# Kernel tuning notes

Measured on AMD Instinct MI355X. Metric: run time of the kernel, lower is better.

## Reference

```python
import jax, jax.numpy as jnp
import numpy as np

BLOCK = 64  # bnb 4-bit quant block size along the input dim

def dequant4bit(q, scale):
    # q: [out, in] int codes in [0,16); scale: [out, in//BLOCK]
    # symmetric 4-bit dequant: w = (code - 7.5) * blockwise scale
    return (q.astype(jnp.float32) - 7.5) * jnp.repeat(scale, BLOCK, axis=1)

def setup_inputs() -> dict:
    key = jax.random.key(0)
    ks = jax.random.split(key, 11)
    B, S, D, H, R = 4, 2048, 2048, 8192, 16
    return {
        "x1": jax.random.normal(ks[0], (B, S, D), jnp.float32),
        "w_up_q": jax.random.randint(ks[1], (H, D), 0, 16, dtype=jnp.int32),
        "w_up_scale": jax.random.uniform(ks[2], (H, D // BLOCK), jnp.float32) * 0.02,
        "b_up": jax.random.normal(ks[3], (H,), jnp.float32) * 0.01,
        "w_up_lora_a": jax.random.normal(ks[4], (D, R), jnp.float32) * 0.02,
        "w_up_lora_b": jax.random.normal(ks[5], (R, H), jnp.float32) * 0.02,
        "w_down_q": jax.random.randint(ks[6], (D, H), 0, 16, dtype=jnp.int32),
        "w_down_scale": jax.random.uniform(ks[7], (D, H // BLOCK), jnp.float32) * 0.02,
        "b_down": jax.random.normal(ks[8], (D,), jnp.float32) * 0.01,
        "w_down_lora_a": jax.random.normal(ks[9], (H, R), jnp.float32) * 0.02,
        "w_down_lora_b": jax.random.normal(ks[10], (R, D), jnp.float32) * 0.02,
    }

def reference(x1, w_up_q, w_up_scale, b_up, w_up_lora_a, w_up_lora_b,
              w_down_q, w_down_scale, b_down, w_down_lora_a, w_down_lora_b):
    # up projection: dequant-matmul + bias + LoRA (activation_forward='relu')
    w_up = dequant4bit(w_up_q, w_up_scale).T            # [D, H]
    y1 = x1 @ w_up + b_up + (x1 @ w_up_lora_a) @ w_up_lora_b   # [B, S, H]
    x2 = jax.nn.relu(y1)
    # down projection: dequant-matmul + bias + LoRA
    w_down = dequant4bit(w_down_q, w_down_scale).T      # [H, D]
    y2 = x2 @ w_down + b_down + (x2 @ w_down_lora_a) @ w_down_lora_b  # [B, S, D]
    return y2
```

## Files before the change

### kernel.cpp

```cpp
#include <hip/hip_runtime.h>
#include <hip/hip_bf16.h>
#include <stdint.h>
#include <stddef.h>

typedef __bf16 bf16;
typedef bf16  bf16x4 __attribute__((ext_vector_type(4)));
typedef bf16  bf16x8 __attribute__((ext_vector_type(8)));
typedef float f32x4  __attribute__((ext_vector_type(4)));

__device__ __forceinline__ void async_copy16(bf16* lds, const bf16* g) {
    __builtin_amdgcn_global_load_lds(
        (const __attribute__((address_space(1))) void*)g,
        (__attribute__((address_space(3))) void*)lds,
        16, 0, 0);
}

__device__ __forceinline__ void bar() { __builtin_amdgcn_s_barrier(); }
#define SFENCE() __builtin_amdgcn_sched_barrier(0)
#define WAIT_VM6()   do { asm volatile("s_waitcnt vmcnt(6)");   SFENCE(); } while (0)
#define WAIT_VM0()   do { asm volatile("s_waitcnt vmcnt(0)");   SFENCE(); } while (0)

__global__ __launch_bounds__(256) void cast_f32_to_bf16(
        const float* __restrict__ in, bf16* __restrict__ out, int n4) {
    int i = blockIdx.x * blockDim.x + threadIdx.x;
    if (i >= n4) return;
    const float4 v = *(const float4*)(in + (size_t)i * 4);
    bf16x4 o;
    o[0] = (bf16)v.x; o[1] = (bf16)v.y; o[2] = (bf16)v.z; o[3] = (bf16)v.w;
    *(bf16x4*)(out + (size_t)i * 4) = o;
}

__global__ __launch_bounds__(256) void dequant_lora(
        const int*   __restrict__ q,
        const float* __restrict__ scale,
        const float* __restrict__ A,
        const float* __restrict__ Bm,
        bf16* __restrict__ out,
        int N, int K) {
    const int tid = threadIdx.x;
    const int k0 = blockIdx.x * 64;
    const int n0 = blockIdx.y * 64;
    const int kk = k0 + (tid & 15) * 4;
    const int nb = n0 + (tid >> 4) * 4;

    f32x4 Ar[4][4];
    #pragma unroll
    for (int i = 0; i < 4; ++i)
        #pragma unroll
        for (int rq = 0; rq < 4; ++rq)
            Ar[i][rq] = *(const f32x4*)&A[(size_t)(kk + i) * 16 + rq * 4];
    f32x4 Br[16];
    #pragma unroll
    for (int r = 0; r < 16; ++r)
        Br[r] = *(const f32x4*)&Bm[(size_t)r * N + nb];

    const int scol = (unsigned)k0 >> 6;
    #pragma unroll
    for (int nn = 0; nn < 4; ++nn) {
        const int n = nb + nn;
        const int4 qv = *(const int4*)&q[(size_t)n * K + kk];
        const float s = scale[(size_t)n * (K >> 6) + scol];
        float l0 = 0.f, l1 = 0.f, l2 = 0.f, l3 = 0.f;
        #pragma unroll
        for (int r = 0; r < 16; ++r) {
            const float bv = Br[r][nn];
            l0 += Ar[0][r >> 2][r & 3] * bv;
            l1 += Ar[1][r >> 2][r & 3] * bv;
            l2 += Ar[2][r >> 2][r & 3] * bv;
            l3 += Ar[3][r >> 2][r & 3] * bv;
        }
        bf16x4 o;
        o[0] = (bf16)(((float)qv.x - 7.5f) * s + l0);
        o[1] = (bf16)(((float)qv.y - 7.5f) * s + l1);
        o[2] = (bf16)(((float)qv.z - 7.5f) * s + l2);
        o[3] = (bf16)(((float)qv.w - 7.5f) * s + l3);
        *(bf16x4*)&out[(size_t)n * K + kk] = o;
    }
}

template <bool RELU, typename OUT_T>
__global__ __launch_bounds__(512, 2) void gemm_bt256(
        const bf16* __restrict__ A, const bf16* __restrict__ B,
        const float* __restrict__ bias, OUT_T* __restrict__ C,
        int M, int N, int K) {
    __shared__ __attribute__((aligned(16))) bf16 As0[2][8192];
    __shared__ __attribute__((aligned(16))) bf16 As1[2][8192];
    __shared__ __attribute__((aligned(16))) bf16 Bs0[2][8192];
    __shared__ __attribute__((aligned(16))) bf16 Bs1[2][8192];

    const int tid  = threadIdx.x;
    const int wave = tid >> 6;
    const int lane = tid & 63;
    const int wm   = wave >> 2;
    const int wn   = wave & 3;
    const int bn   = blockIdx.x;
    const int bm   = blockIdx.y;

    const int srow = tid >> 3;
    const int scol = ((tid & 7) ^ (srow & 7)) * 8;
    const bf16* gA = A + ((size_t)(bm * 256) + srow) * K + scol;
    const bf16* gB = B + ((size_t)(bn * 256) + srow) * K + scol;

    auto stage2 = [&](bf16* halfBase, const bf16* g) {
        bf16* l = halfBase + wave * 512;
        async_copy16(l, g);
        async_copy16(l + 4096, g + (size_t)64 * K);
    };

    const int fr  = lane & 15;
    const int kq  = lane >> 4;
    const int cg0 = ((kq    ) ^ (fr & 7)) * 8;
    const int cg1 = ((kq + 4) ^ (fr & 7)) * 8;
    const int ra  = fr * 64;
    const int rb  = (wn & 1) * 4096 + fr * 64;

    f32x4 acc[8][4];
    #pragma unroll
    for (int i = 0; i < 8; ++i)
        #pragma unroll
        for (int j = 0; j < 4; ++j) {
            f32x4 z = {0.f, 0.f, 0.f, 0.f};
            acc[i][j] = z;
        }

    stage2(&Bs0[0][0], gB);
    stage2(&Bs0[1][0], gB + (size_t)128 * K);
    stage2(&As0[0][0], gA);
    stage2(&As0[1][0], gA + (size_t)128 * K);
    stage2(&Bs1[0][0], gB + 64);
    stage2(&Bs1[1][0], gB + (size_t)128 * K + 64);
    stage2(&As1[0][0], gA + 64);
    WAIT_VM6();
    bar();

    const int NT = K >> 6;
    bf16x8 fa[4][2], fb[4][2];

    for (int t0 = 0; t0 < NT; t0 += 2) {
        #pragma unroll
        for (int u = 0; u < 2; ++u) {
            const int t = t0 + u;
            bf16 (*AsC)[8192] = u ? As1 : As0;
            bf16 (*AsN)[8192] = u ? As0 : As1;
            bf16 (*BsC)[8192] = u ? Bs1 : Bs0;
            const bf16* aC = &AsC[wm][0];
            const bf16* bC = &BsC[wn >> 1][0];

            #pragma unroll
            for (int i = 0; i < 4; ++i) {
                fa[i][0] = *(const bf16x8*)(aC + i * 1024 + ra + cg0);
                fa[i][1] = *(const bf16x8*)(aC + i * 1024 + ra + cg1);
            }
            #pragma unroll
            for (int j = 0; j < 4; ++j) {
                fb[j][0] = *(const bf16x8*)(bC + rb + j * 1024 + cg0);
                fb[j][1] = *(const bf16x8*)(bC + rb + j * 1024 + cg1);
            }
            if (t + 1 < NT)
                stage2(&AsN[1][0], gA + (size_t)128 * K + (size_t)(t + 1) * 64);
            bar();
            __builtin_amdgcn_s_setprio(1);
            #pragma unroll
            for (int ks = 0; ks < 2; ++ks)
                #pragma unroll
                for (int i = 0; i < 4; ++i)
                    #pragma unroll
                    for (int j = 0; j < 2; ++j)
                        acc[i][j] = __builtin_amdgcn_mfma_f32_16x16x32_bf16(
                            fa[i][ks], fb[j][ks], acc[i][j], 0, 0, 0);
            __builtin_amdgcn_s_setprio(0);
            bar();

            if (t + 2 < NT)
                stage2(&BsC[0][0], gB + (size_t)(t + 2) * 64);
            bar();
            __builtin_amdgcn_s_setprio(1);
            #pragma unroll
            for (int ks = 0; ks < 2; ++ks)
                #pragma unroll
                for (int i = 0; i < 4; ++i)
                    #pragma unroll
                    for (int j = 2; j < 4; ++j)
                        acc[i][j] = __builtin_amdgcn_mfma_f32_16x16x32_bf16(
                            fa[i][ks], fb[j][ks], acc[i][j], 0, 0, 0);
            __builtin_amdgcn_s_setprio(0);
            bar();

            #pragma unroll
            for (int i = 0; i < 4; ++i) {
                fa[i][0] = *(const bf16x8*)(aC + (i + 4) * 1024 + ra + cg0);
                fa[i][1] = *(const bf16x8*)(aC + (i + 4) * 1024 + ra + cg1);
            }
            if (t + 2 < NT)
                stage2(&BsC[1][0], gB + (size_t)128 * K + (size_t)(t + 2) * 64);
            bar();
            __builtin_amdgcn_s_setprio(1);
            #pragma unroll
            for (int ks = 0; ks < 2; ++ks)
                #pragma unroll
                for (int i = 0; i < 4; ++i)
                    #pragma unroll
                    for (int j = 2; j < 4; ++j)
                        acc[i + 4][j] = __builtin_amdgcn_mfma_f32_16x16x32_bf16(
                            fa[i][ks], fb[j][ks], acc[i + 4][j], 0, 0, 0);
            __builtin_amdgcn_s_setprio(0);
            bar();

            if (t + 2 < NT) {
                stage2(&AsC[0][0], gA + (size_t)(t + 2) * 64);
                WAIT_VM6();
            } else {
                WAIT_VM0();
            }
            bar();
            __builtin_amdgcn_s_setprio(1);
            #pragma unroll
            for (int ks = 0; ks < 2; ++ks)
                #pragma unroll
                for (int i = 0; i < 4; ++i)
                    #pragma unroll
                    for (int j = 0; j < 2; ++j)
                        acc[i + 4][j] = __builtin_amdgcn_mfma_f32_16x16x32_bf16(
                            fa[i][ks], fb[j][ks], acc[i + 4][j], 0, 0, 0);
            __builtin_amdgcn_s_setprio(0);
            bar();
        }
    }

    const int er = bm * 256 + wm * 128 + (lane >> 4) * 4;
    const int ec = bn * 256 + wn * 64 + fr;
    #pragma unroll
    for (int j = 0; j < 4; ++j) {
        const int col = ec + j * 16;
        const float bv = bias[col];
        #pragma unroll
        for (int i = 0; i < 8; ++i) {
            #pragma unroll
            for (int r = 0; r < 4; ++r) {
                const int row = er + i * 16 + r;
                float v = acc[i][j][r] + bv;
                if (RELU) v = v > 0.f ? v : 0.f;
                C[(size_t)row * N + col] = (OUT_T)v;
            }
        }
    }
}

extern "C" void kernel_launch(void* const* d_in, const int* in_sizes, int n_in,
                              void* d_out, int out_size, void* d_ws, size_t ws_size,
                              hipStream_t stream) {
    const float* x1           = (const float*)d_in[0];
    const int*   w_up_q       = (const int*)  d_in[1];
    const float* w_up_scale   = (const float*)d_in[2];
    const float* b_up         = (const float*)d_in[3];
    const float* w_up_lora_a  = (const float*)d_in[4];
    const float* w_up_lora_b  = (const float*)d_in[5];
    const int*   w_down_q     = (const int*)  d_in[6];
    const float* w_down_scale = (const float*)d_in[7];
    const float* b_down       = (const float*)d_in[8];
    const float* w_down_lora_a= (const float*)d_in[9];
    const float* w_down_lora_b= (const float*)d_in[10];
    float* out = (float*)d_out;

    const int M = 8192, D = 2048, H = 8192;

    char* ws = (char*)d_ws;
    bf16* x1b = (bf16*)ws;
    bf16* wup = (bf16*)(ws + (size_t)M * D * 2);
    bf16* x2  = (bf16*)(ws + (size_t)M * D * 2 + (size_t)H * D * 2);
    bf16* wdn = x1b;

    {
        int n4 = (M * D) / 4;
        cast_f32_to_bf16<<<dim3((n4 + 255) / 256), dim3(256), 0, stream>>>(x1, x1b, n4);
    }
    dequant_lora<<<dim3(D / 64, H / 64), dim3(256), 0, stream>>>(
        w_up_q, w_up_scale, w_up_lora_a, w_up_lora_b, wup, H, D);
    gemm_bt256<true, bf16><<<dim3(H / 256, M / 256), dim3(512), 0, stream>>>(
        x1b, wup, b_up, x2, M, H, D);
    dequant_lora<<<dim3(H / 64, D / 64), dim3(256), 0, stream>>>(
        w_down_q, w_down_scale, w_down_lora_a, w_down_lora_b, wdn, D, H);
    gemm_bt256<false, float><<<dim3(D / 256, M / 256), dim3(512), 0, stream>>>(
        x2, wdn, b_down, out, M, D, H);
}
```

Measured before the change: 757.6 us.

## Restructure GEMM main loop to split K-halves and prefetch next tile fragments

Reorganizes the 8-wave MFMA main loop so each phase computes a full 4x4 sub-block for one K half (cg0 or cg1), using separate register sets rA0/rA1/rB0/rB1. LDS fragment reads for the next phase, and the next tile's first fragments, are issued before the current MFMAs. Global staging is regrouped: both A halves are prefetched one tile ahead and both B halves two tiles ahead, with the wait threshold changed to vmcnt(4). The goal is to hide LDS read latency behind MFMAs and reduce stalls at barriers, at the cost of more live fragment registers and a changed wait and hazard structure.

```diff
diff --git a/kernel.cpp b/kernel.cpp
--- a/kernel.cpp
+++ b/kernel.cpp
@@ -17,8 +17,8 @@
 
 __device__ __forceinline__ void bar() { __builtin_amdgcn_s_barrier(); }
 #define SFENCE() __builtin_amdgcn_sched_barrier(0)
-#define WAIT_VM6()   do { asm volatile("s_waitcnt vmcnt(6)");   SFENCE(); } while (0)
-#define WAIT_VM0()   do { asm volatile("s_waitcnt vmcnt(0)");   SFENCE(); } while (0)
+#define WAIT_VM4() do { asm volatile("s_waitcnt vmcnt(4)"); SFENCE(); } while (0)
+#define WAIT_VM0() do { asm volatile("s_waitcnt vmcnt(0)"); SFENCE(); } while (0)
 
 __global__ __launch_bounds__(256) void cast_f32_to_bf16(
         const float* __restrict__ in, bf16* __restrict__ out, int n4) {
@@ -123,18 +123,28 @@
             acc[i][j] = z;
         }
 
+    stage2(&As0[0][0], gA);
+    stage2(&As0[1][0], gA + (size_t)128 * K);
     stage2(&Bs0[0][0], gB);
     stage2(&Bs0[1][0], gB + (size_t)128 * K);
-    stage2(&As0[0][0], gA);
-    stage2(&As0[1][0], gA + (size_t)128 * K);
     stage2(&Bs1[0][0], gB + 64);
     stage2(&Bs1[1][0], gB + (size_t)128 * K + 64);
-    stage2(&As1[0][0], gA + 64);
-    WAIT_VM6();
+    WAIT_VM4();
     bar();
 
     const int NT = K >> 6;
-    bf16x8 fa[4][2], fb[4][2];
+    bf16x8 rA0[4], rA1[4], rB0[4], rB1[4];
+
+    {
+        const bf16* aC = &As0[wm][0];
+        const bf16* bC = &Bs0[wn >> 1][0];
+        #pragma unroll
+        for (int i = 0; i < 4; ++i)
+            rA0[i] = *(const bf16x8*)(aC + i * 1024 + ra + cg0);
+        #pragma unroll
+        for (int j = 0; j < 4; ++j)
+            rB0[j] = *(const bf16x8*)(bC + rb + j * 1024 + cg0);
+    }
 
     for (int t0 = 0; t0 < NT; t0 += 2) {
         #pragma unroll
@@ -143,85 +153,84 @@
             bf16 (*AsC)[8192] = u ? As1 : As0;
             bf16 (*AsN)[8192] = u ? As0 : As1;
             bf16 (*BsC)[8192] = u ? Bs1 : Bs0;
+            bf16 (*BsN)[8192] = u ? Bs0 : Bs1;
             const bf16* aC = &AsC[wm][0];
             const bf16* bC = &BsC[wn >> 1][0];
-
-            #pragma unroll
-            for (int i = 0; i < 4; ++i) {
-                fa[i][0] = *(const bf16x8*)(aC + i * 1024 + ra + cg0);
-                fa[i][1] = *(const bf16x8*)(aC + i * 1024 + ra + cg1);
-            }
-            #pragma unroll
-            for (int j = 0; j < 4; ++j) {
-                fb[j][0] = *(const bf16x8*)(bC + rb + j * 1024 + cg0);
-                fb[j][1] = *(const bf16x8*)(bC + rb + j * 1024 + cg1);
-            }
-            if (t + 1 < NT)
+            const bf16* aN = &AsN[wm][0];
+            const bf16* bN = &BsN[wn >> 1][0];
+
+            if (t + 1 < NT) {
+                stage2(&AsN[0][0], gA + (size_t)(t + 1) * 64);
                 stage2(&AsN[1][0], gA + (size_t)128 * K + (size_t)(t + 1) * 64);
-            bar();
-            __builtin_amdgcn_s_setprio(1);
-            #pragma unroll
-            for (int ks = 0; ks < 2; ++ks)
+            }
+            #pragma unroll
+            for (int i = 0; i < 4; ++i)
+                rA1[i] = *(const bf16x8*)(aC + (i + 4) * 1024 + ra + cg0);
+            bar();
+            __builtin_amdgcn_s_setprio(1);
+            #pragma unroll
+            for (int i = 0; i < 4; ++i)
+                #pragma unroll
+                for (int j = 0; j < 4; ++j)
+                    acc[i][j] = __builtin_amdgcn_mfma_f32_16x16x32_bf16(
+                        rA0[i], rB0[j], acc[i][j], 0, 0, 0);
+            __builtin_amdgcn_s_setprio(0);
+            bar();
+
+            #pragma unroll
+            for (int i = 0; i < 4; ++i)
+                rA0[i] = *(const bf16x8*)(aC + i * 1024 + ra + cg1);
+            #pragma unroll
+            for (int j = 0; j < 4; ++j)
+                rB1[j] = *(const bf16x8*)(bC + rb + j * 1024 + cg1);
+            bar();
+            __builtin_amdgcn_s_setprio(1);
+            #pragma unroll
+            for (int i = 0; i < 4; ++i)
+                #pragma unroll
+                for (int j = 0; j < 4; ++j)
+                    acc[i + 4][j] = __builtin_amdgcn_mfma_f32_16x16x32_bf16(
+                        rA1[i], rB0[j], acc[i + 4][j], 0, 0, 0);
+            __builtin_amdgcn_s_setprio(0);
+            bar();
+
+            #pragma unroll
+            for (int i = 0; i < 4; ++i)
+                rA1[i] = *(const bf16x8*)(aC + (i + 4) * 1024 + ra + cg1);
+            bar();
+            __builtin_amdgcn_s_setprio(1);
+            #pragma unroll
+            for (int i = 0; i < 4; ++i)
+                #pragma unroll
+                for (int j = 0; j < 4; ++j)
+                    acc[i][j] = __builtin_amdgcn_mfma_f32_16x16x32_bf16(
+                        rA0[i], rB1[j], acc[i][j], 0, 0, 0);
+            __builtin_amdgcn_s_setprio(0);
+            bar();
+
+            if (t + 2 < NT) {
+                stage2(&BsC[0][0], gB + (size_t)(t + 2) * 64);
+                stage2(&BsC[1][0], gB + (size_t)128 * K + (size_t)(t + 2) * 64);
+                WAIT_VM4();
+            } else if (t + 1 < NT) {
+                WAIT_VM0();
+            }
+            bar();
+            if (t + 1 < NT) {
                 #pragma unroll
                 for (int i = 0; i < 4; ++i)
-                    #pragma unroll
-                    for (int j = 0; j < 2; ++j)
-                        acc[i][j] = __builtin_amdgcn_mfma_f32_16x16x32_bf16(
-                            fa[i][ks], fb[j][ks], acc[i][j], 0, 0, 0);
-            __builtin_amdgcn_s_setprio(0);
-            bar();
-
-            if (t + 2 < NT)
-                stage2(&BsC[0][0], gB + (size_t)(t + 2) * 64);
-            bar();
-            __builtin_amdgcn_s_setprio(1);
-            #pragma unroll
-            for (int ks = 0; ks < 2; ++ks)
-                #pragma unroll
-                for (int i = 0; i < 4; ++i)
-                    #pragma unroll
-                    for (int j = 2; j < 4; ++j)
-                        acc[i][j] = __builtin_amdgcn_mfma_f32_16x16x32_bf16(
-                            fa[i][ks], fb[j][ks], acc[i][j], 0, 0, 0);
-            __builtin_amdgcn_s_setprio(0);
-            bar();
-
-            #pragma unroll
-            for (int i = 0; i < 4; ++i) {
-                fa[i][0] = *(const bf16x8*)(aC + (i + 4) * 1024 + ra + cg0);
-                fa[i][1] = *(const bf16x8*)(aC + (i + 4) * 1024 + ra + cg1);
-            }
-            if (t + 2 < NT)
-                stage2(&BsC[1][0], gB + (size_t)128 * K + (size_t)(t + 2) * 64);
-            bar();
-            __builtin_amdgcn_s_setprio(1);
-            #pragma unroll
-            for (int ks = 0; ks < 2; ++ks)
-                #pragma unroll
-                for (int i = 0; i < 4; ++i)
-                    #pragma unroll
-                    for (int j = 2; j < 4; ++j)
-                        acc[i + 4][j] = __builtin_amdgcn_mfma_f32_16x16x32_bf16(
-                            fa[i][ks], fb[j][ks], acc[i + 4][j], 0, 0, 0);
-            __builtin_amdgcn_s_setprio(0);
-            bar();
-
-            if (t + 2 < NT) {
-                stage2(&AsC[0][0], gA + (size_t)(t + 2) * 64);
-                WAIT_VM6();
-            } else {
-                WAIT_VM0();
-            }
-            bar();
-            __builtin_amdgcn_s_setprio(1);
-            #pragma unroll
-            for (int ks = 0; ks < 2; ++ks)
-                #pragma unroll
-                for (int i = 0; i < 4; ++i)
-                    #pragma unroll
-                    for (int j = 0; j < 2; ++j)
-                        acc[i + 4][j] = __builtin_amdgcn_mfma_f32_16x16x32_bf16(
-                            fa[i][ks], fb[j][ks], acc[i + 4][j], 0, 0, 0);
+                    rA0[i] = *(const bf16x8*)(aN + i * 1024 + ra + cg0);
+                #pragma unroll
+                for (int j = 0; j < 4; ++j)
+                    rB0[j] = *(const bf16x8*)(bN + rb + j * 1024 + cg0);
+            }
+            __builtin_amdgcn_s_setprio(1);
+            #pragma unroll
+            for (int i = 0; i < 4; ++i)
+                #pragma unroll
+                for (int j = 0; j < 4; ++j)
+                    acc[i + 4][j] = __builtin_amdgcn_mfma_f32_16x16x32_bf16(
+                        rA1[i], rB1[j], acc[i + 4][j], 0, 0, 0);
             __builtin_amdgcn_s_setprio(0);
             bar();
         }
```

Result: slower. 1.042 ms (+37.6%).
